# Optimization experiments

Hardware: AMD Instinct MI355X
Metric: run time of the kernel (lower is better)

The kernel has to match this reference:

```python
import jax, jax.numpy as jnp
import numpy as np

B, N = 4096, 128


def setup_inputs() -> dict:
    key = jax.random.key(0)
    X = jax.random.normal(key, (B, N, N), dtype=jnp.float32)
    # SPD batch: X X^T / N + eps*I guarantees strictly positive eigenvalues
    spd = jnp.einsum('bij,bkj->bik', X, X) / N + 1e-3 * jnp.eye(N, dtype=jnp.float32)[None]
    return {"input": spd}


def reference(input) -> jnp.ndarray:
    # Batched eigendecomposition (symmetric input -> eigh), then v @ diag(log e) @ v^T
    e, v = jnp.linalg.eigh(input)          # e: [B, N], v: [B, N, N]
    return jnp.einsum('bij,bj,bkj->bik', v, jnp.log(e), v)
```

## Files before the change

kernel.cpp:

```cpp
#include <hip/hip_runtime.h>
#include <hip/hip_bf16.h>
#include <math.h>

#define NM   128
#define PAD  132
#define PB   136
#define PBI  144

typedef __attribute__((ext_vector_type(8))) short bf16x8;
typedef __attribute__((ext_vector_type(4))) float f32x4;
typedef __attribute__((ext_vector_type(4))) int   i32x4;


__global__ __launch_bounds__(256,1)
void scale_kernel(const float* __restrict__ A, float* __restrict__ outY,
                  float* __restrict__ outM, float* __restrict__ lns)
{
    __shared__ __align__(16) float L[NM][PAD];
    __shared__ float rs[NM];
    __shared__ float s_inv;
    const int t = threadIdx.x;
    const long long b = blockIdx.x;
    const long long off = b << 14;
    for (int v = 0; v < 16; ++v) {
        int f = t + v*256;
        int row = f >> 5, c4 = (f & 31) << 2;
        *(float4*)&L[row][c4] = ((const float4*)(A + off))[f];
    }
    __syncthreads();
    if (t < NM) {
        float s = 0.f;
        for (int j = 0; j < NM; ++j) s += fabsf(L[t][j]);
        rs[t] = s;
    }
    __syncthreads();
    if (t < 64) {
        float m = fmaxf(rs[t], rs[t+64]);
        #pragma unroll
        for (int o = 32; o > 0; o >>= 1) m = fmaxf(m, __shfl_down(m, o, 64));
        if (t == 0) { s_inv = 1.0f/m; lns[b] = logf(m); }
    }
    __syncthreads();
    const float inv = s_inv;
    for (int v = 0; v < 16; ++v) {
        int f = t + v*256;
        int row = f >> 5, c4 = (f & 31) << 2;
        float4 x = *(const float4*)&L[row][c4];
        x.x *= inv; x.y *= inv; x.z *= inv; x.w *= inv;
        ((float4*)(outY + off))[f] = x;
        ((float4*)(outM + off))[f] = x;
    }
}

__global__ __launch_bounds__(256,1)
void rescale_kernel(const float* __restrict__ Sq, float* __restrict__ X,
                    float* __restrict__ M, float* __restrict__ lns)
{
    __shared__ __align__(16) float L[NM][PAD];
    __shared__ float rs[NM];
    __shared__ float s_g;
    const int t = threadIdx.x;
    const long long b = blockIdx.x;
    const long long off = b << 14;
    for (int v = 0; v < 16; ++v) {
        int f = t + v*256;
        int row = f >> 5, c4 = (f & 31) << 2;
        *(float4*)&L[row][c4] = ((const float4*)(Sq + off))[f];
    }
    __syncthreads();
    if (t < NM) {
        float s = 0.f;
        for (int j = 0; j < NM; ++j) s += fabsf(L[t][j]);
        rs[t] = s;
    }
    __syncthreads();
    if (t < 64) {
        float m = fmaxf(rs[t], rs[t+64]);
        #pragma unroll
        for (int o = 32; o > 0; o >>= 1) m = fmaxf(m, __shfl_down(m, o, 64));
        if (t == 0) { s_g = 1.0f/sqrtf(m); lns[b] = lns[b] + 0.5f*logf(m); }
    }
    __syncthreads();
    const float g = s_g;
    for (int v = 0; v < 16; ++v) {
        int f = t + v*256;
        float4 x = ((const float4*)(X + off))[f];
        x.x *= g; x.y *= g; x.z *= g; x.w *= g;
        ((float4*)(X + off))[f] = x;
        ((float4*)(M + off))[f] = x;
    }
}

__device__ __forceinline__ void tridec(int u, int &bi, int &bj) {
    int b = (int)(0.5f*(sqrtf(8.0f*(float)u + 1.0f) - 1.0f));
    while ((b+1)*(b+2)/2 <= u) ++b;
    while (b*(b+1)/2 > u) --b;
    bi = b; bj = u - b*(b+1)/2;
}

__global__ __launch_bounds__(512,1)
void gram_tri(const float* __restrict__ X, float* __restrict__ Out)
{
    __shared__ __align__(16) float LX[NM][PAD];
    const int t = threadIdx.x;
    const long long off = (long long)blockIdx.x << 14;
    for (int v = 0; v < 8; ++v) {
        int f = t + v*512;
        int row = f >> 5, c4 = (f & 31) << 2;
        *(float4*)&LX[row][c4] = ((const float4*)(X + off))[f];
    }
    __syncthreads();
    for (int u = t; u < 528; u += 512) {
        int bi, bj; tridec(u, bi, bj);
        const int r4 = bi << 2, c4 = bj << 2;
        float acc[4][4];
        #pragma unroll
        for (int i = 0; i < 4; ++i)
            #pragma unroll
            for (int j = 0; j < 4; ++j) acc[i][j] = 0.f;
        #pragma unroll 4
        for (int k = 0; k < NM; ++k) {
            float av[4], bv[4];
            *(float4*)av = *(const float4*)&LX[k][r4];
            *(float4*)bv = *(const float4*)&LX[k][c4];
            #pragma unroll
            for (int i = 0; i < 4; ++i)
                #pragma unroll
                for (int j = 0; j < 4; ++j) acc[i][j] = fmaf(av[i], bv[j], acc[i][j]);
        }
        #pragma unroll
        for (int i = 0; i < 4; ++i)
            *(float4*)&Out[off + (long long)(r4+i)*NM + c4] =
                make_float4(acc[i][0], acc[i][1], acc[i][2], acc[i][3]);
        if (bi != bj) {
            #pragma unroll
            for (int j = 0; j < 4; ++j)
                *(float4*)&Out[off + (long long)(c4+j)*NM + r4] =
                    make_float4(acc[0][j], acc[1][j], acc[2][j], acc[3][j]);
        }
    }
}

__device__ __forceinline__ f32x4 mfma16(bf16x8 a, bf16x8 b, f32x4 c) {
    return __builtin_amdgcn_mfma_f32_16x16x32_bf16(a, b, c, 0, 0, 0);
}

__device__ __forceinline__ void splitbf(float x, unsigned short &h, unsigned short &l) {
    __hip_bfloat16 bh = __float2bfloat16(x);
    float r = x - __bfloat162float(bh);
    __hip_bfloat16 bl = __float2bfloat16(r);
    h = *(unsigned short*)&bh;
    l = *(unsigned short*)&bl;
}

__device__ __forceinline__ float ldsM(const unsigned short* __restrict__ H,
                                      const unsigned short* __restrict__ L,
                                      int row, int col) {
    unsigned int uh = ((unsigned int)H[row*PB + col]) << 16;
    unsigned int ul = ((unsigned int)L[row*PB + col]) << 16;
    return __uint_as_float(uh) + __uint_as_float(ul);
}

__device__ __forceinline__ bf16x8 ldfrag(const unsigned short* __restrict__ a,
                                         int rb, int lane, int kc) {
    int row = rb*16 + (lane & 15);
    int col = kc*32 + ((lane >> 4) & 3)*8;
    return *(const bf16x8*)(a + row*PB + col);
}

__device__ __forceinline__ f32x4 symdiag(f32x4 a, int lane) {
    const int g = (lane >> 4) & 3, j = lane & 15;
    const int rp = j & 3;
    f32x4 out;
    #pragma unroll
    for (int r = 0; r < 4; ++r) {
        int lp = 4*g + r + ((j >> 2) << 4);
        float t0 = __shfl(a[0], lp, 64);
        float t1 = __shfl(a[1], lp, 64);
        float t2 = __shfl(a[2], lp, 64);
        float t3 = __shfl(a[3], lp, 64);
        float tv = (rp == 0) ? t0 : (rp == 1) ? t1 : (rp == 2) ? t2 : t3;
        out[r] = 0.5f*(a[r] + tv);
    }
    return out;
}

__device__ __forceinline__ void st_split(unsigned short* __restrict__ H,
                                         unsigned short* __restrict__ L,
                                         int Tr, int Tc, int lane, f32x4 o) {
    int col = Tc*16 + (lane & 15);
    int rb  = Tr*16 + ((lane >> 4) & 3)*4;
    #pragma unroll
    for (int r = 0; r < 4; ++r) {
        unsigned short h, l;
        splitbf(o[r], h, l);
        H[(rb+r)*PB + col] = h;
        L[(rb+r)*PB + col] = l;
        if (Tr != Tc) { H[col*PB + rb + r] = h; L[col*PB + rb + r] = l; }
    }
}

__device__ __forceinline__ void stg_sym(float* __restrict__ out, long long off,
                                        int Tr, int Tc, int lane, f32x4 o) {
    int col = Tc*16 + (lane & 15);
    int rb  = Tr*16 + ((lane >> 4) & 3)*4;
    #pragma unroll
    for (int r = 0; r < 4; ++r)
        out[off + (long long)(rb+r)*NM + col] = o[r];
    if (Tr != Tc)
        *(f32x4*)&out[off + (long long)col*NM + rb] = o;
}

__device__ __forceinline__ f32x4 yepi(const unsigned short* __restrict__ Yh,
                                      const unsigned short* __restrict__ Yl,
                                      int Tr, int Tc, int lane, f32x4 a,
                                      float a15, float a05) {
    int col = Tc*16 + (lane & 15);
    int rb  = Tr*16 + ((lane >> 4) & 3)*4;
    f32x4 o;
    #pragma unroll
    for (int r = 0; r < 4; ++r)
        o[r] = a15*ldsM(Yh, Yl, rb+r, col) - a05*a[r];
    if (Tr == Tc) o = symdiag(o, lane);
    return o;
}

__device__ __forceinline__ f32x4 mepi(const unsigned short* __restrict__ Mh,
                                      const unsigned short* __restrict__ Ml,
                                      const unsigned short* __restrict__ Th,
                                      const unsigned short* __restrict__ Tl,
                                      int Tr, int Tc, int lane, f32x4 a, float q) {
    int col = Tc*16 + (lane & 15);
    int rb  = Tr*16 + ((lane >> 4) & 3)*4;
    f32x4 o;
    #pragma unroll
    for (int r = 0; r < 4; ++r)
        o[r] = q*(9.f*ldsM(Mh, Ml, rb+r, col) - 6.f*ldsM(Th, Tl, rb+r, col) + a[r]);
    if (Tr == Tc) o = symdiag(o, lane);
    return o;
}

__device__ __forceinline__ f32x4 pepi(const unsigned short* __restrict__ Ph,
                                      const unsigned short* __restrict__ Pl,
                                      int Tr, int Tc, int lane, f32x4 a,
                                      float s1, float s2, float dadd) {
    int col = Tc*16 + (lane & 15);
    int rb  = Tr*16 + ((lane >> 4) & 3)*4;
    f32x4 o;
    #pragma unroll
    for (int r = 0; r < 4; ++r)
        o[r] = s1*a[r] - s2*ldsM(Ph, Pl, rb+r, col) + ((rb+r) == col ? dadd : 0.f);
    if (Tr == Tc) o = symdiag(o, lane);
    return o;
}

template<int W>
struct TS16 {
    static constexpr int P  = W >> 2;
    static constexpr int Q  = W & 3;
    static constexpr int R0 = P;
    static constexpr int R1 = 7 - P;
    static constexpr int N  = (Q == 0) ? 3 : 2;
    static constexpr int g(int i)  { return 4*i + Q; }
    static constexpr int tr(int i) { return g(i) <= R0 ? R0 : R1; }
    static constexpr int tc(int i) { return g(i) <= R0 ? g(i) : g(i) - R0 - 1; }
};

template<int W>
__device__ __forceinline__ void tri16_gemm(const unsigned short* __restrict__ Ah,
                                           const unsigned short* __restrict__ Al,
                                           const unsigned short* __restrict__ Bh,
                                           const unsigned short* __restrict__ Bl,
                                           int lane, f32x4* acc) {
    using TS = TS16<W>;
    #pragma unroll
    for (int kc = 0; kc < 4; ++kc) {
        bf16x8 a0h = ldfrag(Ah, TS::R0, lane, kc), a0l = ldfrag(Al, TS::R0, lane, kc);
        bf16x8 a1h = ldfrag(Ah, TS::R1, lane, kc), a1l = ldfrag(Al, TS::R1, lane, kc);
        #pragma unroll
        for (int i = 0; i < TS::N; ++i) {
            const int r = TS::tr(i), c = TS::tc(i);
            bf16x8 bh = ldfrag(Bh, c, lane, kc), bl = ldfrag(Bl, c, lane, kc);
            bf16x8 ah = (r == TS::R0) ? a0h : a1h;
            bf16x8 al = (r == TS::R0) ? a0l : a1l;
            acc[i] = mfma16(ah, bh, acc[i]);
            acc[i] = mfma16(ah, bl, acc[i]);
            acc[i] = mfma16(al, bh, acc[i]);
        }
    }
}

template<int W>
__device__ __forceinline__ void ns_fused_body16(
    unsigned short* Mh, unsigned short* Ml,
    unsigned short* Yh, unsigned short* Yl,
    float* outY, long long off, int lane, int niter)
{
    using TS = TS16<W>;
    constexpr int NT_ = TS::N;
    const f32x4 z = {0.f, 0.f, 0.f, 0.f};
    f32x4 acc[NT_], yv[NT_];

    for (int j = 0; j < niter; ++j) {
        const int last = (j == niter-1);
        const float cc = (j < niter-3) ? 1.5f : ((j == niter-3) ? 1.116f : 1.0f);
        const float dd = sqrtf(cc);
        const float a15 = 1.5f*dd, a05 = 0.5f*dd;

        #pragma unroll
        for (int i = 0; i < NT_; ++i) acc[i] = z;
        tri16_gemm<W>(Yh, Yl, Mh, Ml, lane, acc);
        #pragma unroll
        for (int i = 0; i < NT_; ++i)
            yv[i] = yepi(Yh, Yl, TS::tr(i), TS::tc(i), lane, acc[i], a15, a05);

        if (last) {
            #pragma unroll
            for (int i = 0; i < NT_; ++i)
                stg_sym(outY, off, TS::tr(i), TS::tc(i), lane, yv[i]);
            return;
        }
        __syncthreads();

        #pragma unroll
        for (int i = 0; i < NT_; ++i) acc[i] = z;
        tri16_gemm<W>(Mh, Ml, Mh, Ml, lane, acc);
        #pragma unroll
        for (int i = 0; i < NT_; ++i)
            st_split(Yh, Yl, TS::tr(i), TS::tc(i), lane, acc[i]);
        __syncthreads();

        #pragma unroll
        for (int i = 0; i < NT_; ++i) acc[i] = z;
        tri16_gemm<W>(Mh, Ml, Yh, Yl, lane, acc);
        const float q = 0.25f*cc;
        #pragma unroll
        for (int i = 0; i < NT_; ++i)
            acc[i] = mepi(Mh, Ml, Yh, Yl, TS::tr(i), TS::tc(i), lane, acc[i], q);
        __syncthreads();

        #pragma unroll
        for (int i = 0; i < NT_; ++i)
            st_split(Mh, Ml, TS::tr(i), TS::tc(i), lane, acc[i]);
        #pragma unroll
        for (int i = 0; i < NT_; ++i)
            st_split(Yh, Yl, TS::tr(i), TS::tc(i), lane, yv[i]);
        __syncthreads();
    }
}

__global__ __launch_bounds__(1024,1)
void ns_fused(const float* __restrict__ Mp, const float* __restrict__ Yp,
              float* __restrict__ outY, int niter)
{
    __shared__ __align__(16) unsigned short pool[4*NM*PB];
    unsigned short* Mh = pool;
    unsigned short* Ml = pool + NM*PB;
    unsigned short* Yh = pool + 2*NM*PB;
    unsigned short* Yl = pool + 3*NM*PB;

    const int t = threadIdx.x;
    const long long off = (long long)blockIdx.x << 14;
    for (int v = 0; v < 4; ++v) {
        int f = t + v*1024;
        int row = f >> 5, c4 = (f & 31) << 2;
        float4 x = ((const float4*)(Mp + off))[f];
        ushort4 h, l;
        splitbf(x.x, h.x, l.x); splitbf(x.y, h.y, l.y);
        splitbf(x.z, h.z, l.z); splitbf(x.w, h.w, l.w);
        *(ushort4*)&Mh[row*PB + c4] = h;
        *(ushort4*)&Ml[row*PB + c4] = l;
        x = ((const float4*)(Yp + off))[f];
        splitbf(x.x, h.x, l.x); splitbf(x.y, h.y, l.y);
        splitbf(x.z, h.z, l.z); splitbf(x.w, h.w, l.w);
        *(ushort4*)&Yh[row*PB + c4] = h;
        *(ushort4*)&Yl[row*PB + c4] = l;
    }
    __syncthreads();

    const int lane = t & 63;
    const int w = t >> 6;
    switch (w) {
        case 0:  ns_fused_body16<0>(Mh,Ml,Yh,Yl,outY,off,lane,niter); break;
        case 1:  ns_fused_body16<1>(Mh,Ml,Yh,Yl,outY,off,lane,niter); break;
        case 2:  ns_fused_body16<2>(Mh,Ml,Yh,Yl,outY,off,lane,niter); break;
        case 3:  ns_fused_body16<3>(Mh,Ml,Yh,Yl,outY,off,lane,niter); break;
        case 4:  ns_fused_body16<4>(Mh,Ml,Yh,Yl,outY,off,lane,niter); break;
        case 5:  ns_fused_body16<5>(Mh,Ml,Yh,Yl,outY,off,lane,niter); break;
        case 6:  ns_fused_body16<6>(Mh,Ml,Yh,Yl,outY,off,lane,niter); break;
        case 7:  ns_fused_body16<7>(Mh,Ml,Yh,Yl,outY,off,lane,niter); break;
        case 8:  ns_fused_body16<8>(Mh,Ml,Yh,Yl,outY,off,lane,niter); break;
        case 9:  ns_fused_body16<9>(Mh,Ml,Yh,Yl,outY,off,lane,niter); break;
        case 10: ns_fused_body16<10>(Mh,Ml,Yh,Yl,outY,off,lane,niter); break;
        case 11: ns_fused_body16<11>(Mh,Ml,Yh,Yl,outY,off,lane,niter); break;
        case 12: ns_fused_body16<12>(Mh,Ml,Yh,Yl,outY,off,lane,niter); break;
        case 13: ns_fused_body16<13>(Mh,Ml,Yh,Yl,outY,off,lane,niter); break;
        case 14: ns_fused_body16<14>(Mh,Ml,Yh,Yl,outY,off,lane,niter); break;
        default: ns_fused_body16<15>(Mh,Ml,Yh,Yl,outY,off,lane,niter); break;
    }
}

struct PolyCoefs {
    float a, bd;
    float s1, s2;
    float c0,c1,c2,c3,c4,c5;
    float f1, f2, f3;
};

template<int W>
__device__ __forceinline__ void poly_fused_body16(
    const unsigned short* Xh, const unsigned short* Xl,
    unsigned short* Ph, unsigned short* Pl,
    float* Out, long long off, int lane, PolyCoefs pc, float lnsb)
{
    using TS = TS16<W>;
    constexpr int NT_ = TS::N;
    const f32x4 z = {0.f, 0.f, 0.f, 0.f};
    f32x4 acc[NT_];

    for (int step = 0; step < 6; ++step) {
        #pragma unroll
        for (int i = 0; i < NT_; ++i) acc[i] = z;
        tri16_gemm<W>(Xh, Xl, Ph, Pl, lane, acc);
        float s3v;
        switch (step) {
            case 0: s3v = pc.c0; break;  case 1: s3v = pc.c1; break;
            case 2: s3v = pc.c2; break;  case 3: s3v = pc.c3; break;
            case 4: s3v = pc.c4; break;  default: s3v = pc.c5; break;
        }
        #pragma unroll
        for (int i = 0; i < NT_; ++i)
            acc[i] = pepi(Ph, Pl, TS::tr(i), TS::tc(i), lane, acc[i], pc.s1, pc.s2, s3v);
        __syncthreads();
        #pragma unroll
        for (int i = 0; i < NT_; ++i)
            st_split(Ph, Pl, TS::tr(i), TS::tc(i), lane, acc[i]);
        __syncthreads();
    }
    #pragma unroll
    for (int i = 0; i < NT_; ++i) acc[i] = z;
    tri16_gemm<W>(Xh, Xl, Ph, Pl, lane, acc);
    const float dadd = pc.f3 + lnsb;
    #pragma unroll
    for (int i = 0; i < NT_; ++i) {
        f32x4 o = pepi(Ph, Pl, TS::tr(i), TS::tc(i), lane, acc[i], pc.f1, pc.f2, dadd);
        stg_sym(Out, off, TS::tr(i), TS::tc(i), lane, o);
    }
}

__global__ __launch_bounds__(1024,1)
void poly_fused(const float* __restrict__ Xp, float* __restrict__ Out,
                const float* __restrict__ lns, PolyCoefs pc)
{
    __shared__ __align__(16) unsigned short pool[4*NM*PB];
    unsigned short* Xh = pool;
    unsigned short* Xl = pool + NM*PB;
    unsigned short* Ph = pool + 2*NM*PB;
    unsigned short* Pl = pool + 3*NM*PB;

    const int t = threadIdx.x;
    const long long b = blockIdx.x;
    const long long off = b << 14;
    for (int v = 0; v < 4; ++v) {
        int f = t + v*1024;
        int row = f >> 5, c4 = (f & 31) << 2;
        float4 x = ((const float4*)(Xp + off))[f];
        float4 p;
        p.x = pc.a*x.x + ((c4+0)==row ? pc.bd : 0.f);
        p.y = pc.a*x.y + ((c4+1)==row ? pc.bd : 0.f);
        p.z = pc.a*x.z + ((c4+2)==row ? pc.bd : 0.f);
        p.w = pc.a*x.w + ((c4+3)==row ? pc.bd : 0.f);
        ushort4 h, l;
        splitbf(x.x, h.x, l.x); splitbf(x.y, h.y, l.y);
        splitbf(x.z, h.z, l.z); splitbf(x.w, h.w, l.w);
        *(ushort4*)&Xh[row*PB + c4] = h;
        *(ushort4*)&Xl[row*PB + c4] = l;
        splitbf(p.x, h.x, l.x); splitbf(p.y, h.y, l.y);
        splitbf(p.z, h.z, l.z); splitbf(p.w, h.w, l.w);
        *(ushort4*)&Ph[row*PB + c4] = h;
        *(ushort4*)&Pl[row*PB + c4] = l;
    }
    __syncthreads();

    const float lnsb = lns[b];
    const int lane = t & 63;
    const int w = t >> 6;
    switch (w) {
        case 0:  poly_fused_body16<0>(Xh,Xl,Ph,Pl,Out,off,lane,pc,lnsb); break;
        case 1:  poly_fused_body16<1>(Xh,Xl,Ph,Pl,Out,off,lane,pc,lnsb); break;
        case 2:  poly_fused_body16<2>(Xh,Xl,Ph,Pl,Out,off,lane,pc,lnsb); break;
        case 3:  poly_fused_body16<3>(Xh,Xl,Ph,Pl,Out,off,lane,pc,lnsb); break;
        case 4:  poly_fused_body16<4>(Xh,Xl,Ph,Pl,Out,off,lane,pc,lnsb); break;
        case 5:  poly_fused_body16<5>(Xh,Xl,Ph,Pl,Out,off,lane,pc,lnsb); break;
        case 6:  poly_fused_body16<6>(Xh,Xl,Ph,Pl,Out,off,lane,pc,lnsb); break;
        case 7:  poly_fused_body16<7>(Xh,Xl,Ph,Pl,Out,off,lane,pc,lnsb); break;
        case 8:  poly_fused_body16<8>(Xh,Xl,Ph,Pl,Out,off,lane,pc,lnsb); break;
        case 9:  poly_fused_body16<9>(Xh,Xl,Ph,Pl,Out,off,lane,pc,lnsb); break;
        case 10: poly_fused_body16<10>(Xh,Xl,Ph,Pl,Out,off,lane,pc,lnsb); break;
        case 11: poly_fused_body16<11>(Xh,Xl,Ph,Pl,Out,off,lane,pc,lnsb); break;
        case 12: poly_fused_body16<12>(Xh,Xl,Ph,Pl,Out,off,lane,pc,lnsb); break;
        case 13: poly_fused_body16<13>(Xh,Xl,Ph,Pl,Out,off,lane,pc,lnsb); break;
        case 14: poly_fused_body16<14>(Xh,Xl,Ph,Pl,Out,off,lane,pc,lnsb); break;
        default: poly_fused_body16<15>(Xh,Xl,Ph,Pl,Out,off,lane,pc,lnsb); break;
    }
}

__device__ __forceinline__ i32x4 mfma8(i32x4 a, i32x4 b, i32x4 c) {
    return __builtin_amdgcn_mfma_i32_16x16x64_i8(a, b, c, 0, 0, 0);
}

__device__ __forceinline__ void spliti(float x, int &h, int &m, int &l) {
    int xi = __float2int_rn(x * 2097152.0f);
    l = (int)(signed char)(xi & 255);
    int r1 = (xi - l) >> 8;
    m = (int)(signed char)(r1 & 255);
    h = (r1 - m) >> 8;
}

__device__ __forceinline__ void pack4i(float4 x, unsigned &uh, unsigned &um, unsigned &ul) {
    float v[4] = {x.x, x.y, x.z, x.w};
    uh = um = ul = 0;
    #pragma unroll
    for (int i = 0; i < 4; ++i) {
        int h, m, l;
        spliti(v[i], h, m, l);
        uh |= ((unsigned)(h & 255)) << (8*i);
        um |= ((unsigned)(m & 255)) << (8*i);
        ul |= ((unsigned)(l & 255)) << (8*i);
    }
}

__device__ __forceinline__ float recLDS(const signed char* __restrict__ H,
                                        const signed char* __restrict__ Md,
                                        const signed char* __restrict__ L,
                                        int row, int col) {
    int v = ((int)H[row*PBI + col] << 16) + ((int)Md[row*PBI + col] << 8)
          + (int)L[row*PBI + col];
    return (float)v * 4.76837158203125e-7f;
}

__device__ __forceinline__ f32x4 rec4(i32x4 g0, i32x4 g1, i32x4 g2, i32x4 g3) {
    f32x4 r;
    #pragma unroll
    for (int i = 0; i < 4; ++i)
        r[i] = (float)g0[i]*9.765625e-4f
             + (float)g1[i]*3.814697265625e-6f
             + (float)g2[i]*1.4901161193847656e-8f
             + (float)g3[i]*5.8207660913467407e-11f;
    return r;
}

__device__ __forceinline__ i32x4 ldfrag8(const signed char* __restrict__ p,
                                         int rb, int lane, int kc) {
    int row = rb*16 + (lane & 15);
    int col = kc*64 + ((lane >> 4) & 3)*16;
    return *(const i32x4*)(p + row*PBI + col);
}

__device__ __forceinline__ void st_packed(signed char* __restrict__ H,
                                          signed char* __restrict__ Md,
                                          signed char* __restrict__ L,
                                          int Tr, int Tc, int lane,
                                          unsigned yh, unsigned ym, unsigned yl) {
    int col = Tc*16 + (lane & 15);
    int rb  = Tr*16 + ((lane >> 4) & 3)*4;
    #pragma unroll
    for (int r = 0; r < 4; ++r) {
        signed char h = (signed char)((yh >> (8*r)) & 255);
        signed char m = (signed char)((ym >> (8*r)) & 255);
        signed char l = (signed char)((yl >> (8*r)) & 255);
        H[(rb+r)*PBI + col] = h;
        Md[(rb+r)*PBI + col] = m;
        L[(rb+r)*PBI + col] = l;
        if (Tr != Tc) {
            H[col*PBI + rb + r] = h;
            Md[col*PBI + rb + r] = m;
            L[col*PBI + rb + r] = l;
        }
    }
}

__device__ __forceinline__ void st_spliti(signed char* __restrict__ H,
                                          signed char* __restrict__ Md,
                                          signed char* __restrict__ L,
                                          int Tr, int Tc, int lane, f32x4 o) {
    int col = Tc*16 + (lane & 15);
    int rb  = Tr*16 + ((lane >> 4) & 3)*4;
    #pragma unroll
    for (int r = 0; r < 4; ++r) {
        int h, m, l;
        spliti(o[r], h, m, l);
        H[(rb+r)*PBI + col] = (signed char)h;
        Md[(rb+r)*PBI + col] = (signed char)m;
        L[(rb+r)*PBI + col] = (signed char)l;
        if (Tr != Tc) {
            H[col*PBI + rb + r] = (signed char)h;
            Md[col*PBI + rb + r] = (signed char)m;
            L[col*PBI + rb + r] = (signed char)l;
        }
    }
}

__device__ __forceinline__ void tile_gemm_i8(
    const signed char* __restrict__ Ah, const signed char* __restrict__ Am,
    const signed char* __restrict__ Al,
    const signed char* __restrict__ Bh, const signed char* __restrict__ Bm,
    const signed char* __restrict__ Bl,
    int r, int c, int lane,
    i32x4 &g0, i32x4 &g1, i32x4 &g2, i32x4 &g3)
{
    #pragma unroll
    for (int kc = 0; kc < 2; ++kc) {
        i32x4 ah = ldfrag8(Ah, r, lane, kc);
        i32x4 am = ldfrag8(Am, r, lane, kc);
        i32x4 al = ldfrag8(Al, r, lane, kc);
        i32x4 bh = ldfrag8(Bh, c, lane, kc);
        i32x4 bm = ldfrag8(Bm, c, lane, kc);
        i32x4 bl = ldfrag8(Bl, c, lane, kc);
        g0 = mfma8(ah, bh, g0);
        g1 = mfma8(ah, bm, g1);
        g1 = mfma8(am, bh, g1);
        g2 = mfma8(ah, bl, g2);
        g2 = mfma8(am, bm, g2);
        g2 = mfma8(al, bh, g2);
        g3 = mfma8(am, bl, g3);
        g3 = mfma8(al, bm, g3);
    }
}

template<int W>
__device__ __forceinline__ void ns_i8_body16(
    signed char* Mh, signed char* Mm, signed char* Ml,
    signed char* Yh, signed char* Ym, signed char* Yl,
    float* outM, float* outY, long long off, int lane, int niter)
{
    using TS = TS16<W>;
    constexpr int NT_ = TS::N;
    const i32x4 zi = {0, 0, 0, 0};
    unsigned yph[NT_], ypm[NT_], ypl[NT_];
    const float cc = 1.5f, dd = sqrtf(1.5f);
    const float a15 = 1.5f*dd, a05 = 0.5f*dd, q = 0.25f*cc;

    for (int j = 0; j < niter; ++j) {
        const int last = (j == niter-1);

        #pragma unroll
        for (int i = 0; i < NT_; ++i) {
            const int Tr = TS::tr(i), Tc = TS::tc(i);
            i32x4 g0 = zi, g1 = zi, g2 = zi, g3 = zi;
            tile_gemm_i8(Yh,Ym,Yl, Mh,Mm,Ml, Tr, Tc, lane, g0,g1,g2,g3);
            f32x4 a = rec4(g0, g1, g2, g3);
            int col = Tc*16 + (lane & 15);
            int rb  = Tr*16 + ((lane >> 4) & 3)*4;
            f32x4 o;
            #pragma unroll
            for (int r = 0; r < 4; ++r)
                o[r] = a15*recLDS(Yh, Ym, Yl, rb+r, col) - a05*a[r];
            if (Tr == Tc) o = symdiag(o, lane);
            if (last) {
                stg_sym(outY, off, Tr, Tc, lane, o);
            } else {
                float4 of = make_float4(o[0], o[1], o[2], o[3]);
                pack4i(of, yph[i], ypm[i], ypl[i]);
            }
        }
        __syncthreads();

        #pragma unroll
        for (int i = 0; i < NT_; ++i) {
            const int Tr = TS::tr(i), Tc = TS::tc(i);
            i32x4 g0 = zi, g1 = zi, g2 = zi, g3 = zi;
            tile_gemm_i8(Mh,Mm,Ml, Mh,Mm,Ml, Tr, Tc, lane, g0,g1,g2,g3);
            f32x4 tv = rec4(g0, g1, g2, g3);
            st_spliti(Yh, Ym, Yl, Tr, Tc, lane, tv);
        }
        __syncthreads();

        if (last) {
            #pragma unroll
            for (int i = 0; i < NT_; ++i) {
                const int Tr = TS::tr(i), Tc = TS::tc(i);
                i32x4 g0 = zi, g1 = zi, g2 = zi, g3 = zi;
                tile_gemm_i8(Mh,Mm,Ml, Yh,Ym,Yl, Tr, Tc, lane, g0,g1,g2,g3);
                f32x4 a = rec4(g0, g1, g2, g3);
                int col = Tc*16 + (lane & 15);
                int rb  = Tr*16 + ((lane >> 4) & 3)*4;
                f32x4 o;
                #pragma unroll
                for (int r = 0; r < 4; ++r)
                    o[r] = q*(9.f*recLDS(Mh, Mm, Ml, rb+r, col)
                            - 6.f*recLDS(Yh, Ym, Yl, rb+r, col) + a[r]);
                if (Tr == Tc) o = symdiag(o, lane);
                stg_sym(outM, off, Tr, Tc, lane, o);
            }
            return;
        }
        {
            f32x4 mv[NT_];
            #pragma unroll
            for (int i = 0; i < NT_; ++i) {
                const int Tr = TS::tr(i), Tc = TS::tc(i);
                i32x4 g0 = zi, g1 = zi, g2 = zi, g3 = zi;
                tile_gemm_i8(Mh,Mm,Ml, Yh,Ym,Yl, Tr, Tc, lane, g0,g1,g2,g3);
                f32x4 a = rec4(g0, g1, g2, g3);
                int col = Tc*16 + (lane & 15);
                int rb  = Tr*16 + ((lane >> 4) & 3)*4;
                f32x4 o;
                #pragma unroll
                for (int r = 0; r < 4; ++r)
                    o[r] = q*(9.f*recLDS(Mh, Mm, Ml, rb+r, col)
                            - 6.f*recLDS(Yh, Ym, Yl, rb+r, col) + a[r]);
                if (Tr == Tc) o = symdiag(o, lane);
                mv[i] = o;
            }
            __syncthreads();
            #pragma unroll
            for (int i = 0; i < NT_; ++i)
                st_spliti(Mh, Mm, Ml, TS::tr(i), TS::tc(i), lane, mv[i]);
            #pragma unroll
            for (int i = 0; i < NT_; ++i)
                st_packed(Yh, Ym, Yl, TS::tr(i), TS::tc(i), lane,
                          yph[i], ypm[i], ypl[i]);
            __syncthreads();
        }
    }
}

__global__ __launch_bounds__(1024,4)
void ns_i8(const float* __restrict__ Mp, const float* __restrict__ Yp,
           float* __restrict__ outM, float* __restrict__ outY, int niter)
{
    __shared__ __align__(16) signed char pool8[6*NM*PBI];
    signed char* Mh = pool8;
    signed char* Mm = pool8 + 1*NM*PBI;
    signed char* Ml = pool8 + 2*NM*PBI;
    signed char* Yh = pool8 + 3*NM*PBI;
    signed char* Ym = pool8 + 4*NM*PBI;
    signed char* Yl = pool8 + 5*NM*PBI;

    const int t = threadIdx.x;
    const long long off = (long long)blockIdx.x << 14;
    for (int v = 0; v < 4; ++v) {
        int f = t + v*1024;
        int row = f >> 5, c4 = (f & 31) << 2;
        unsigned uh, um, ul;
        float4 x = ((const float4*)(Mp + off))[f];
        pack4i(x, uh, um, ul);
        *(unsigned*)&Mh[row*PBI + c4] = uh;
        *(unsigned*)&Mm[row*PBI + c4] = um;
        *(unsigned*)&Ml[row*PBI + c4] = ul;
        x = ((const float4*)(Yp + off))[f];
        pack4i(x, uh, um, ul);
        *(unsigned*)&Yh[row*PBI + c4] = uh;
        *(unsigned*)&Ym[row*PBI + c4] = um;
        *(unsigned*)&Yl[row*PBI + c4] = ul;
    }
    __syncthreads();

    const int lane = t & 63;
    const int w = t >> 6;
    switch (w) {
        case 0:  ns_i8_body16<0>(Mh,Mm,Ml,Yh,Ym,Yl,outM,outY,off,lane,niter); break;
        case 1:  ns_i8_body16<1>(Mh,Mm,Ml,Yh,Ym,Yl,outM,outY,off,lane,niter); break;
        case 2:  ns_i8_body16<2>(Mh,Mm,Ml,Yh,Ym,Yl,outM,outY,off,lane,niter); break;
        case 3:  ns_i8_body16<3>(Mh,Mm,Ml,Yh,Ym,Yl,outM,outY,off,lane,niter); break;
        case 4:  ns_i8_body16<4>(Mh,Mm,Ml,Yh,Ym,Yl,outM,outY,off,lane,niter); break;
        case 5:  ns_i8_body16<5>(Mh,Mm,Ml,Yh,Ym,Yl,outM,outY,off,lane,niter); break;
        case 6:  ns_i8_body16<6>(Mh,Mm,Ml,Yh,Ym,Yl,outM,outY,off,lane,niter); break;
        case 7:  ns_i8_body16<7>(Mh,Mm,Ml,Yh,Ym,Yl,outM,outY,off,lane,niter); break;
        case 8:  ns_i8_body16<8>(Mh,Mm,Ml,Yh,Ym,Yl,outM,outY,off,lane,niter); break;
        case 9:  ns_i8_body16<9>(Mh,Mm,Ml,Yh,Ym,Yl,outM,outY,off,lane,niter); break;
        case 10: ns_i8_body16<10>(Mh,Mm,Ml,Yh,Ym,Yl,outM,outY,off,lane,niter); break;
        case 11: ns_i8_body16<11>(Mh,Mm,Ml,Yh,Ym,Yl,outM,outY,off,lane,niter); break;
        case 12: ns_i8_body16<12>(Mh,Mm,Ml,Yh,Ym,Yl,outM,outY,off,lane,niter); break;
        case 13: ns_i8_body16<13>(Mh,Mm,Ml,Yh,Ym,Yl,outM,outY,off,lane,niter); break;
        case 14: ns_i8_body16<14>(Mh,Mm,Ml,Yh,Ym,Yl,outM,outY,off,lane,niter); break;
        default: ns_i8_body16<15>(Mh,Mm,Ml,Yh,Ym,Yl,outM,outY,off,lane,niter); break;
    }
}

#define LDA  129
#define NT   512
#define MAX_SWEEPS 14

__global__ __launch_bounds__(NT, 1)
void logeig_jacobi(const float* __restrict__ in, float* __restrict__ out)
{
    __shared__ float A[NM][LDA];
    __shared__ float V[NM][LDA];
    __shared__ float rc[64], rs[64];
    __shared__ float logd[NM];
    __shared__ float roff[NT/64], rdia[NT/64];
    __shared__ int   s_done;

    const int t = threadIdx.x;
    const long long b = blockIdx.x;
    const float* __restrict__ Ain  = in  + (b << 14);
    float* __restrict__       Aout = out + (b << 14);

    for (int k = 0; k < (NM*NM)/NT; ++k) {
        int idx = t + k*NT;
        int i = idx >> 7, j = idx & 127;
        A[i][j] = Ain[idx];
        V[i][j] = (i == j) ? 1.0f : 0.0f;
    }
    __syncthreads();

    for (int sweep = 0; sweep < MAX_SWEEPS; ++sweep) {
        for (int r = 0; r < NM-1; ++r) {
            if (t < 64) {
                int m = t, p, q;
                if (m == 0) { p = NM-1; q = r; }
                else {
                    p = r + m;            if (p >= NM-1) p -= (NM-1);
                    q = r - m + (NM-1);   if (q >= NM-1) q -= (NM-1);
                }
                float app = A[p][p], aqq = A[q][q], apq = A[p][q];
                float c = 1.0f, s = 0.0f;
                if (fabsf(apq) > 1e-12f*(fabsf(app)+fabsf(aqq)) + 1e-32f) {
                    float tau = (aqq - app) * 0.5f / apq;
                    float tt  = 1.0f / (fabsf(tau) + sqrtf(fmaf(tau,tau,1.0f)));
                    tt = (tau < 0.0f) ? -tt : tt;
                    c = rsqrtf(fmaf(tt,tt,1.0f));
                    s = tt * c;
                }
                rc[m] = c; rs[m] = s;
            }
            __syncthreads();
            for (int k = 0; k < (2*64*NM)/NT; ++k) {
                int task = t + k*NT;
                int i   = task & 127;
                int m   = (task >> 7) & 63;
                int isV = task >> 13;
                int p, q;
                if (m == 0) { p = NM-1; q = r; }
                else {
                    p = r + m;            if (p >= NM-1) p -= (NM-1);
                    q = r - m + (NM-1);   if (q >= NM-1) q -= (NM-1);
                }
                float c = rc[m], s = rs[m];
                if (isV == 0) {
                    float x = A[i][p], y = A[i][q];
                    A[i][p] = c*x - s*y;
                    A[i][q] = s*x + c*y;
                } else {
                    float x = V[i][p], y = V[i][q];
                    V[i][p] = c*x - s*y;
                    V[i][q] = s*x + c*y;
                }
            }
            __syncthreads();
            for (int k = 0; k < (64*NM)/NT; ++k) {
                int task = t + k*NT;
                int j = task & 127;
                int m = task >> 7;
                int p, q;
                if (m == 0) { p = NM-1; q = r; }
                else {
                    p = r + m;            if (p >= NM-1) p -= (NM-1);
                    q = r - m + (NM-1);   if (q >= NM-1) q -= (NM-1);
                }
                float c = rc[m], s = rs[m];
                float x = A[p][j], y = A[q][j];
                A[p][j] = c*x - s*y;
                A[q][j] = s*x + c*y;
            }
            __syncthreads();
        }
        float off2 = 0.0f, dia2 = 0.0f;
        for (int k = 0; k < (NM*NM)/NT; ++k) {
            int idx = t + k*NT;
            int i = idx >> 7, j = idx & 127;
            float v = A[i][j];
            if (i == j) dia2 += v*v; else off2 += v*v;
        }
        #pragma unroll
        for (int o = 32; o > 0; o >>= 1) {
            off2 += __shfl_down(off2, o, 64);
            dia2 += __shfl_down(dia2, o, 64);
        }
        if ((t & 63) == 0) { roff[t >> 6] = off2; rdia[t >> 6] = dia2; }
        __syncthreads();
        if (t == 0) {
            float o2 = 0.0f, d2 = 0.0f;
            for (int w = 0; w < NT/64; ++w) { o2 += roff[w]; d2 += rdia[w]; }
            s_done = (o2 <= 1e-13f * d2) ? 1 : 0;
        }
        __syncthreads();
        if (s_done) break;
    }

    if (t < NM) logd[t] = logf(fmaxf(A[t][t], 1e-12f));
    __syncthreads();
    for (int kk = 0; kk < (NM*NM)/NT; ++kk) {
        int idx = t + kk*NT;
        int i = idx >> 7, k = idx & 127;
        A[i][k] = V[i][k] * logd[k];
    }
    __syncthreads();
    {
        int i  = t >> 2;
        int jb = t & 3;
        float acc[32];
        #pragma unroll
        for (int jj = 0; jj < 32; ++jj) acc[jj] = 0.0f;
        for (int kk = 0; kk < NM; ++kk) {
            int k = (kk + jb) & 127;
            float w = A[i][k];
            #pragma unroll
            for (int jj = 0; jj < 32; ++jj)
                acc[jj] = fmaf(w, V[jb*32 + jj][k], acc[jj]);
        }
        #pragma unroll
        for (int jj = 0; jj < 32; ++jj)
            Aout[i*NM + jb*32 + jj] = acc[jj];
    }
}

static void cheb_log_power(double lo, double up, int deg, double* p)
{
    const int NC = deg + 1;
    const int MN = 64;
    double mid = 0.5*(lo+up), hw = 0.5*(up-lo);
    double cc[32];
    for (int j = 0; j < NC; ++j) {
        double s = 0.0;
        for (int m = 0; m < MN; ++m) {
            double th = M_PI*(m+0.5)/MN;
            s += log(mid + hw*cos(th)) * cos(j*th);
        }
        cc[j] = 2.0*s/MN;
    }
    double Tp[32] = {0}, Tc[32] = {0}, Tn[32];
    for (int j = 0; j < NC; ++j) p[j] = 0.0;
    Tp[0] = 1.0;  p[0] += 0.5*cc[0];
    Tc[1] = 1.0;  p[1] += cc[1];
    for (int k = 2; k <= deg; ++k) {
        for (int j = 0; j < NC; ++j) Tn[j] = -Tp[j];
        for (int j = 1; j < NC; ++j) Tn[j] += 2.0*Tc[j-1];
        for (int j = 0; j < NC; ++j) { p[j] += cc[k]*Tn[j]; Tp[j] = Tc[j]; Tc[j] = Tn[j]; }
    }
}

extern "C" void kernel_launch(void* const* d_in, const int* in_sizes, int n_in,
                              void* d_out, int out_size, void* d_ws, size_t ws_size,
                              hipStream_t stream) {
    const float* in = (const float*)d_in[0];
    float* out = (float*)d_out;
    const int batch = in_sizes[0] >> 14;
    const size_t matBytes = (size_t)batch * NM * NM * 4;
    const size_t need = matBytes + (size_t)batch * 4;

    if (ws_size < need) {
        logeig_jacobi<<<batch, NT, 0, stream>>>(in, out);
        return;
    }

    float* Mbuf = (float*)d_ws;
    float* lns  = (float*)((char*)d_ws + matBytes);

    scale_kernel<<<batch, 256, 0, stream>>>(in, out, Mbuf, lns);
    gram_tri<<<batch, 512, 0, stream>>>(out, Mbuf);
    rescale_kernel<<<batch, 256, 0, stream>>>(Mbuf, out, Mbuf, lns);

    ns_i8<<<batch, 1024, 0, stream>>>(Mbuf, out, Mbuf, out, 4);

    ns_fused<<<batch, 1024, 0, stream>>>(Mbuf, out, out, 8);
    ns_fused<<<batch, 1024, 0, stream>>>(out,  out, out, 8);
    ns_fused<<<batch, 1024, 0, stream>>>(out,  out, out, 6);

    const double lo = 0.25, up = 1.002;
    const double mid = 0.5*(lo+up), hw = 0.5*(up-lo);
    double p[9];
    cheb_log_power(lo, up, 8, p);

    PolyCoefs pc;
    pc.a  = (float)(p[8]/hw);
    pc.bd = (float)(p[7] - p[8]*mid/hw);
    pc.s1 = (float)(1.0/hw);
    pc.s2 = (float)(mid/hw);
    pc.c0 = (float)p[6]; pc.c1 = (float)p[5]; pc.c2 = (float)p[4];
    pc.c3 = (float)p[3]; pc.c4 = (float)p[2]; pc.c5 = (float)p[1];
    pc.f1 = (float)(8.0/hw);
    pc.f2 = (float)(8.0*mid/hw);
    pc.f3 = (float)(8.0*p[0]);

    poly_fused<<<batch, 1024, 0, stream>>>(out, out, lns, pc);
}
```

Before: 6.042 ms.

## Run int8 Newton-Schulz kernel with 8 waves, two tile pairs per wave

The int8 Newton-Schulz kernel drops from 16 waves (1024 threads) to 8 waves (512 threads), and each wave now handles twice as many lower-triangular 16x16 tiles through a new TS8 tile schedule. The new M values are packed to split int8 in registers before the barrier and stored with st_packed, rather than held as floats and split after the barrier. The aim is to cut per-block thread count and barrier cost and to shorten the window between barriers. The trade is more register pressure and fewer waves to hide LDS and MFMA latency. Launch bounds change from (1024,4) to (512,1).

```diff
diff --git a/kernel.cpp b/kernel.cpp
--- a/kernel.cpp
+++ b/kernel.cpp
@@ -264,6 +264,17 @@
     static constexpr int g(int i)  { return 4*i + Q; }
     static constexpr int tr(int i) { return g(i) <= R0 ? R0 : R1; }
     static constexpr int tc(int i) { return g(i) <= R0 ? g(i) : g(i) - R0 - 1; }
+};
+
+template<int W>
+struct TS8 {
+    static constexpr int P  = W & 3;
+    static constexpr int R0 = P;
+    static constexpr int R1 = 7 - P;
+    static constexpr int H  = W >> 2;
+    static constexpr int N  = (10 - H) / 2;
+    static constexpr int tr(int i) { int g = 2*i + H; return g <= R0 ? R0 : R1; }
+    static constexpr int tc(int i) { int g = 2*i + H; return g <= R0 ? g : g - R0 - 1; }
 };
 
 template<int W>
@@ -629,15 +640,16 @@
 }
 
 template<int W>
-__device__ __forceinline__ void ns_i8_body16(
+__device__ __forceinline__ void ns_i8_body8(
     signed char* Mh, signed char* Mm, signed char* Ml,
     signed char* Yh, signed char* Ym, signed char* Yl,
     float* outM, float* outY, long long off, int lane, int niter)
 {
-    using TS = TS16<W>;
+    using TS = TS8<W>;
     constexpr int NT_ = TS::N;
     const i32x4 zi = {0, 0, 0, 0};
     unsigned yph[NT_], ypm[NT_], ypl[NT_];
+    unsigned mph[NT_], mpm[NT_], mpl[NT_];
     const float cc = 1.5f, dd = sqrtf(1.5f);
     const float a15 = 1.5f*dd, a05 = 0.5f*dd, q = 0.25f*cc;
 
@@ -695,38 +707,38 @@
             }
             return;
         }
-        {
-            f32x4 mv[NT_];
+        #pragma unroll
+        for (int i = 0; i < NT_; ++i) {
+            const int Tr = TS::tr(i), Tc = TS::tc(i);
+            i32x4 g0 = zi, g1 = zi, g2 = zi, g3 = zi;
+            tile_gemm_i8(Mh,Mm,Ml, Yh,Ym,Yl, Tr, Tc, lane, g0,g1,g2,g3);
+            f32x4 a = rec4(g0, g1, g2, g3);
+            int col = Tc*16 + (lane & 15);
+            int rb  = Tr*16 + ((lane >> 4) & 3)*4;
+            f32x4 o;
             #pragma unroll
-            for (int i = 0; i < NT_; ++i) {
-                const int Tr = TS::tr(i), Tc = TS::tc(i);
-                i32x4 g0 = zi, g1 = zi, g2 = zi, g3 = zi;
-                tile_gemm_i8(Mh,Mm,Ml, Yh,Ym,Yl, Tr, Tc, lane, g0,g1,g2,g3);
-                f32x4 a = rec4(g0, g1, g2, g3);
-                int col = Tc*16 + (lane & 15);
-                int rb  = Tr*16 + ((lane >> 4) & 3)*4;
-                f32x4 o;
-                #pragma unroll
-                for (int r = 0; r < 4; ++r)
-                    o[r] = q*(9.f*recLDS(Mh, Mm, Ml, rb+r, col)
-                            - 6.f*recLDS(Yh, Ym, Yl, rb+r, col) + a[r]);
-                if (Tr == Tc) o = symdiag(o, lane);
-                mv[i] = o;
-            }
-            __syncthreads();
-            #pragma unroll
-            for (int i = 0; i < NT_; ++i)
-                st_spliti(Mh, Mm, Ml, TS::tr(i), TS::tc(i), lane, mv[i]);
-            #pragma unroll
-            for (int i = 0; i < NT_; ++i)
-                st_packed(Yh, Ym, Yl, TS::tr(i), TS::tc(i), lane,
-                          yph[i], ypm[i], ypl[i]);
-            __syncthreads();
-        }
-    }
-}
-
-__global__ __launch_bounds__(1024,4)
+            for (int r = 0; r < 4; ++r)
+                o[r] = q*(9.f*recLDS(Mh, Mm, Ml, rb+r, col)
+                        - 6.f*recLDS(Yh, Ym, Yl, rb+r, col) + a[r]);
+            if (Tr == Tc) o = symdiag(o, lane);
+            float4 of = make_float4(o[0], o[1], o[2], o[3]);
+            pack4i(of, mph[i], mpm[i], mpl[i]);
+        }
+        __syncthreads();
+
+        #pragma unroll
+        for (int i = 0; i < NT_; ++i)
+            st_packed(Mh, Mm, Ml, TS::tr(i), TS::tc(i), lane,
+                      mph[i], mpm[i], mpl[i]);
+        #pragma unroll
+        for (int i = 0; i < NT_; ++i)
+            st_packed(Yh, Ym, Yl, TS::tr(i), TS::tc(i), lane,
+                      yph[i], ypm[i], ypl[i]);
+        __syncthreads();
+    }
+}
+
+__global__ __launch_bounds__(512,1)
 void ns_i8(const float* __restrict__ Mp, const float* __restrict__ Yp,
            float* __restrict__ outM, float* __restrict__ outY, int niter)
 {
@@ -740,8 +752,8 @@
 
     const int t = threadIdx.x;
     const long long off = (long long)blockIdx.x << 14;
-    for (int v = 0; v < 4; ++v) {
-        int f = t + v*1024;
+    for (int v = 0; v < 8; ++v) {
+        int f = t + v*512;
         int row = f >> 5, c4 = (f & 31) << 2;
         unsigned uh, um, ul;
         float4 x = ((const float4*)(Mp + off))[f];
@@ -760,22 +772,14 @@
     const int lane = t & 63;
     const int w = t >> 6;
     switch (w) {
-        case 0:  ns_i8_body16<0>(Mh,Mm,Ml,Yh,Ym,Yl,outM,outY,off,lane,niter); break;
-        case 1:  ns_i8_body16<1>(Mh,Mm,Ml,Yh,Ym,Yl,outM,outY,off,lane,niter); break;
-        case 2:  ns_i8_body16<2>(Mh,Mm,Ml,Yh,Ym,Yl,outM,outY,off,lane,niter); break;
-        case 3:  ns_i8_body16<3>(Mh,Mm,Ml,Yh,Ym,Yl,outM,outY,off,lane,niter); break;
-        case 4:  ns_i8_body16<4>(Mh,Mm,Ml,Yh,Ym,Yl,outM,outY,off,lane,niter); break;
-        case 5:  ns_i8_body16<5>(Mh,Mm,Ml,Yh,Ym,Yl,outM,outY,off,lane,niter); break;
-        case 6:  ns_i8_body16<6>(Mh,Mm,Ml,Yh,Ym,Yl,outM,outY,off,lane,niter); break;
-        case 7:  ns_i8_body16<7>(Mh,Mm,Ml,Yh,Ym,Yl,outM,outY,off,lane,niter); break;
-        case 8:  ns_i8_body16<8>(Mh,Mm,Ml,Yh,Ym,Yl,outM,outY,off,lane,niter); break;
-        case 9:  ns_i8_body16<9>(Mh,Mm,Ml,Yh,Ym,Yl,outM,outY,off,lane,niter); break;
-        case 10: ns_i8_body16<10>(Mh,Mm,Ml,Yh,Ym,Yl,outM,outY,off,lane,niter); break;
-        case 11: ns_i8_body16<11>(Mh,Mm,Ml,Yh,Ym,Yl,outM,outY,off,lane,niter); break;
-        case 12: ns_i8_body16<12>(Mh,Mm,Ml,Yh,Ym,Yl,outM,outY,off,lane,niter); break;
-        case 13: ns_i8_body16<13>(Mh,Mm,Ml,Yh,Ym,Yl,outM,outY,off,lane,niter); break;
-        case 14: ns_i8_body16<14>(Mh,Mm,Ml,Yh,Ym,Yl,outM,outY,off,lane,niter); break;
-        default: ns_i8_body16<15>(Mh,Mm,Ml,Yh,Ym,Yl,outM,outY,off,lane,niter); break;
+        case 0:  ns_i8_body8<0>(Mh,Mm,Ml,Yh,Ym,Yl,outM,outY,off,lane,niter); break;
+        case 1:  ns_i8_body8<1>(Mh,Mm,Ml,Yh,Ym,Yl,outM,outY,off,lane,niter); break;
+        case 2:  ns_i8_body8<2>(Mh,Mm,Ml,Yh,Ym,Yl,outM,outY,off,lane,niter); break;
+        case 3:  ns_i8_body8<3>(Mh,Mm,Ml,Yh,Ym,Yl,outM,outY,off,lane,niter); break;
+        case 4:  ns_i8_body8<4>(Mh,Mm,Ml,Yh,Ym,Yl,outM,outY,off,lane,niter); break;
+        case 5:  ns_i8_body8<5>(Mh,Mm,Ml,Yh,Ym,Yl,outM,outY,off,lane,niter); break;
+        case 6:  ns_i8_body8<6>(Mh,Mm,Ml,Yh,Ym,Yl,outM,outY,off,lane,niter); break;
+        default: ns_i8_body8<7>(Mh,Mm,Ml,Yh,Ym,Yl,outM,outY,off,lane,niter); break;
     }
 }
 
@@ -963,7 +967,7 @@
     gram_tri<<<batch, 512, 0, stream>>>(out, Mbuf);
     rescale_kernel<<<batch, 256, 0, stream>>>(Mbuf, out, Mbuf, lns);
 
-    ns_i8<<<batch, 1024, 0, stream>>>(Mbuf, out, Mbuf, out, 4);
+    ns_i8<<<batch, 512, 0, stream>>>(Mbuf, out, Mbuf, out, 4);
 
     ns_fused<<<batch, 1024, 0, stream>>>(Mbuf, out, out, 8);
     ns_fused<<<batch, 1024, 0, stream>>>(out,  out, out, 8);
```

Result: slower. 6.239 ms (+3.3%).
